# Kernel tuning notes

Hardware: AMD Instinct MI355X
Metric: run time of the kernel (lower is better)

The kernel has to match this reference:

```python
import jax, jax.numpy as jnp
import numpy as np


def setup_inputs() -> dict:
    key = jax.random.key(0)
    k1, k2, k3 = jax.random.split(key, 3)
    B, N, D = 64, 2048, 1024
    output = jax.random.normal(k1, (B, 1, D), dtype=jnp.float32)
    context = jax.random.normal(k2, (B, N, D), dtype=jnp.float32)
    # nn.Linear(2*dim, dim): weight [dim, 2*dim], bias [dim]
    W_out = jax.random.normal(k3, (D, 2 * D), dtype=jnp.float32) * (1.0 / np.sqrt(2 * D))
    b_out = jnp.zeros((D,), dtype=jnp.float32)
    return {"output": output, "context": context, "W_out": W_out, "b_out": b_out}


def reference(output, context, W_out, b_out):
    B, q, D = output.shape  # q == 1
    N = context.shape[1]
    # scores: (B, q, N) = output @ context^T
    attn = jnp.einsum('bqd,bnd->bqn', output, context)
    attn = jax.nn.softmax(attn, axis=-1)
    # mix: (B, q, D)
    mix = jnp.einsum('bqn,bnd->bqd', attn, context)
    combined = jnp.concatenate([mix, output], axis=-1)  # (B, q, 2D)
    out = jnp.tanh(jnp.einsum('bqe,de->bqd', combined, W_out) + b_out)
    return (out, attn)
```

## Files before the change

kernel.cpp:

```cpp
#include <hip/hip_runtime.h>
#include <cmath>

#define BATCH 64
#define NCTX 2048
#define DIM 1024
#define CHUNKS 16
#define ROWS_PER_CHUNK (NCTX / CHUNKS)
#define ROWS_PER_WAVE (ROWS_PER_CHUNK / 4)

__global__ __launch_bounds__(256) void attn_phase1(
    const float* __restrict__ q,
    const float* __restrict__ ctx,
    float* __restrict__ scores,
    float* __restrict__ part_m,
    float* __restrict__ part_l,
    float* __restrict__ part_o)
{
    const int blk  = blockIdx.x;
    const int b    = blk / CHUNKS;
    const int c    = blk % CHUNKS;
    const int tid  = threadIdx.x;
    const int wave = tid >> 6;
    const int lane = tid & 63;

    float4 qf[4];
    const float* qb = q + (size_t)b * DIM;
    #pragma unroll
    for (int j = 0; j < 4; ++j)
        qf[j] = *reinterpret_cast<const float4*>(qb + lane * 4 + 256 * j);

    float m = -INFINITY, l = 0.f;
    float4 o[4];
    #pragma unroll
    for (int j = 0; j < 4; ++j) o[j] = make_float4(0.f, 0.f, 0.f, 0.f);

    const int row0 = c * ROWS_PER_CHUNK + wave * ROWS_PER_WAVE;
    const float* cb = ctx + (size_t)b * NCTX * DIM;

    for (int i = 0; i < ROWS_PER_WAVE; ++i) {
        const int row = row0 + i;
        const float* cr = cb + (size_t)row * DIM + lane * 4;
        float4 cf[4];
        #pragma unroll
        for (int j = 0; j < 4; ++j)
            cf[j] = *reinterpret_cast<const float4*>(cr + 256 * j);

        float s = 0.f;
        #pragma unroll
        for (int j = 0; j < 4; ++j) {
            s += qf[j].x * cf[j].x;
            s += qf[j].y * cf[j].y;
            s += qf[j].z * cf[j].z;
            s += qf[j].w * cf[j].w;
        }
        #pragma unroll
        for (int off = 32; off >= 1; off >>= 1)
            s += __shfl_xor(s, off, 64);

        if (lane == 0) scores[(size_t)b * NCTX + row] = s;

        const float m_new = fmaxf(m, s);
        const float alpha = __expf(m - m_new);
        const float p     = __expf(s - m_new);
        l = l * alpha + p;
        #pragma unroll
        for (int j = 0; j < 4; ++j) {
            o[j].x = o[j].x * alpha + p * cf[j].x;
            o[j].y = o[j].y * alpha + p * cf[j].y;
            o[j].z = o[j].z * alpha + p * cf[j].z;
            o[j].w = o[j].w * alpha + p * cf[j].w;
        }
        m = m_new;
    }

    __shared__ float wm[4], wl[4];
    __shared__ float o_lds[4 * DIM];
    if (lane == 0) { wm[wave] = m; wl[wave] = l; }
    __syncthreads();

    const float Mb = fmaxf(fmaxf(wm[0], wm[1]), fmaxf(wm[2], wm[3]));
    float Lb = 0.f;
    #pragma unroll
    for (int w = 0; w < 4; ++w) Lb += wl[w] * __expf(wm[w] - Mb);

    const float aw = __expf(m - Mb);
    #pragma unroll
    for (int j = 0; j < 4; ++j) {
        float4 t = o[j];
        t.x *= aw; t.y *= aw; t.z *= aw; t.w *= aw;
        *reinterpret_cast<float4*>(&o_lds[wave * DIM + lane * 4 + 256 * j]) = t;
    }
    __syncthreads();

    {
        const int e = tid * 4;
        float4 s0 = *reinterpret_cast<const float4*>(&o_lds[0 * DIM + e]);
        float4 s1 = *reinterpret_cast<const float4*>(&o_lds[1 * DIM + e]);
        float4 s2 = *reinterpret_cast<const float4*>(&o_lds[2 * DIM + e]);
        float4 s3 = *reinterpret_cast<const float4*>(&o_lds[3 * DIM + e]);
        float4 r;
        r.x = s0.x + s1.x + s2.x + s3.x;
        r.y = s0.y + s1.y + s2.y + s3.y;
        r.z = s0.z + s1.z + s2.z + s3.z;
        r.w = s0.w + s1.w + s2.w + s3.w;
        *reinterpret_cast<float4*>(&part_o[((size_t)b * CHUNKS + c) * DIM + e]) = r;
    }
    if (tid == 0) {
        part_m[b * CHUNKS + c] = Mb;
        part_l[b * CHUNKS + c] = Lb;
    }
}

__global__ __launch_bounds__(256) void attn_phase2(
    const float* __restrict__ scores,
    const float* __restrict__ part_m,
    const float* __restrict__ part_l,
    const float* __restrict__ part_o,
    float* __restrict__ mix,
    float* __restrict__ attn_out)
{
    const int b = blockIdx.x;
    const int tid = threadIdx.x;

    float M = -INFINITY;
    #pragma unroll
    for (int i = 0; i < CHUNKS; ++i) M = fmaxf(M, part_m[b * CHUNKS + i]);

    float w[CHUNKS];
    float L = 0.f;
    #pragma unroll
    for (int i = 0; i < CHUNKS; ++i) {
        w[i] = __expf(part_m[b * CHUNKS + i] - M);
        L += part_l[b * CHUNKS + i] * w[i];
    }
    const float invL = 1.f / L;

    const int e = tid * 4;
    float4 acc = make_float4(0.f, 0.f, 0.f, 0.f);
    #pragma unroll
    for (int i = 0; i < CHUNKS; ++i) {
        float4 t = *reinterpret_cast<const float4*>(
            &part_o[((size_t)b * CHUNKS + i) * DIM + e]);
        acc.x += t.x * w[i];
        acc.y += t.y * w[i];
        acc.z += t.z * w[i];
        acc.w += t.w * w[i];
    }
    acc.x *= invL; acc.y *= invL; acc.z *= invL; acc.w *= invL;
    *reinterpret_cast<float4*>(&mix[(size_t)b * DIM + e]) = acc;

    for (int n = tid; n < NCTX; n += 256)
        attn_out[(size_t)b * NCTX + n] =
            __expf(scores[(size_t)b * NCTX + n] - M) * invL;
}

#define BT 8
#define DT 32
__global__ __launch_bounds__(256) void attn_phase3(
    const float* __restrict__ mix,
    const float* __restrict__ q,
    const float* __restrict__ W,
    const float* __restrict__ bias,
    float* __restrict__ out)
{
    const int d_chunk = blockIdx.x % (DIM / DT);
    const int b_chunk = blockIdx.x / (DIM / DT);
    const int d0 = d_chunk * DT;
    const int b0 = b_chunk * BT;
    const int tid  = threadIdx.x;
    const int wave = tid >> 6;
    const int lane = tid & 63;

    __shared__ float comb[BT * 2 * DIM];
    for (int i = tid; i < BT * 2 * DIM; i += 256) {
        const int bl = i >> 11;
        const int e  = i & 2047;
        comb[i] = (e < DIM) ? mix[(size_t)(b0 + bl) * DIM + e]
                            : q[(size_t)(b0 + bl) * DIM + (e - DIM)];
    }
    __syncthreads();

    const int d_base = d0 + wave * (DT / 4);
    #pragma unroll
    for (int g = 0; g < 2; ++g) {
        const int dg = d_base + g * 4;
        float acc[4][BT];
        #pragma unroll
        for (int di = 0; di < 4; ++di)
            #pragma unroll
            for (int bl = 0; bl < BT; ++bl) acc[di][bl] = 0.f;

        for (int kk = 0; kk < 2 * DIM; kk += 256) {
            float4 wv[4];
            #pragma unroll
            for (int di = 0; di < 4; ++di)
                wv[di] = *reinterpret_cast<const float4*>(
                    W + (size_t)(dg + di) * (2 * DIM) + kk + lane * 4);
            #pragma unroll
            for (int bl = 0; bl < BT; ++bl) {
                float4 cv = *reinterpret_cast<const float4*>(
                    &comb[bl * 2 * DIM + kk + lane * 4]);
                #pragma unroll
                for (int di = 0; di < 4; ++di) {
                    acc[di][bl] += wv[di].x * cv.x;
                    acc[di][bl] += wv[di].y * cv.y;
                    acc[di][bl] += wv[di].z * cv.z;
                    acc[di][bl] += wv[di].w * cv.w;
                }
            }
        }

        float myval = 0.f;
        #pragma unroll
        for (int di = 0; di < 4; ++di) {
            #pragma unroll
            for (int bl = 0; bl < BT; ++bl) {
                float v = acc[di][bl];
                #pragma unroll
                for (int off = 32; off >= 1; off >>= 1)
                    v += __shfl_xor(v, off, 64);
                if (lane == di * BT + bl) myval = v;
            }
        }
        if (lane < 32) {
            const int di = lane >> 3;
            const int bl = lane & 7;
            const int d  = dg + di;
            out[(size_t)(b0 + bl) * DIM + d] = tanhf(myval + bias[d]);
        }
    }
}

extern "C" void kernel_launch(void* const* d_in, const int* in_sizes, int n_in,
                              void* d_out, int out_size, void* d_ws, size_t ws_size,
                              hipStream_t stream) {
    const float* q    = (const float*)d_in[0];
    const float* ctx  = (const float*)d_in[1];
    const float* W    = (const float*)d_in[2];
    const float* bias = (const float*)d_in[3];

    float* out_main = (float*)d_out;
    float* attn_out = (float*)d_out + (size_t)BATCH * DIM;

    float* ws      = (float*)d_ws;
    float* scores  = ws;
    float* part_m  = scores + (size_t)BATCH * NCTX;
    float* part_l  = part_m + BATCH * CHUNKS;
    float* part_o  = part_l + BATCH * CHUNKS;
    float* mix     = part_o + (size_t)BATCH * CHUNKS * DIM;

    attn_phase1<<<BATCH * CHUNKS, 256, 0, stream>>>(q, ctx, scores,
                                                    part_m, part_l, part_o);
    attn_phase2<<<BATCH, 256, 0, stream>>>(scores, part_m, part_l, part_o,
                                           mix, attn_out);
    attn_phase3<<<(DIM / DT) * (BATCH / BT), 256, 0, stream>>>(mix, q, W, bias,
                                                               out_main);
}
```

Before: 713.7 us.

## Process two context rows per iteration, double chunks, shrink phase3 batch tile

```diff
diff --git a/kernel.cpp b/kernel.cpp
--- a/kernel.cpp
+++ b/kernel.cpp
@@ -4,7 +4,7 @@
 #define BATCH 64
 #define NCTX 2048
 #define DIM 1024
-#define CHUNKS 16
+#define CHUNKS 32
 #define ROWS_PER_CHUNK (NCTX / CHUNKS)
 #define ROWS_PER_WAVE (ROWS_PER_CHUNK / 4)
 
@@ -36,41 +36,59 @@
 
     const int row0 = c * ROWS_PER_CHUNK + wave * ROWS_PER_WAVE;
     const float* cb = ctx + (size_t)b * NCTX * DIM;
-
-    for (int i = 0; i < ROWS_PER_WAVE; ++i) {
-        const int row = row0 + i;
-        const float* cr = cb + (size_t)row * DIM + lane * 4;
-        float4 cf[4];
-        #pragma unroll
-        for (int j = 0; j < 4; ++j)
-            cf[j] = *reinterpret_cast<const float4*>(cr + 256 * j);
-
-        float s = 0.f;
+    float* sc = scores + (size_t)b * NCTX;
+
+    for (int i = 0; i < ROWS_PER_WAVE; i += 2) {
+        const int rowA = row0 + i;
+        const int rowB = rowA + 1;
+        const float* crA = cb + (size_t)rowA * DIM + lane * 4;
+        const float* crB = cb + (size_t)rowB * DIM + lane * 4;
+        float4 cfA[4], cfB[4];
         #pragma unroll
         for (int j = 0; j < 4; ++j) {
-            s += qf[j].x * cf[j].x;
-            s += qf[j].y * cf[j].y;
-            s += qf[j].z * cf[j].z;
-            s += qf[j].w * cf[j].w;
-        }
-        #pragma unroll
-        for (int off = 32; off >= 1; off >>= 1)
-            s += __shfl_xor(s, off, 64);
-
-        if (lane == 0) scores[(size_t)b * NCTX + row] = s;
-
-        const float m_new = fmaxf(m, s);
-        const float alpha = __expf(m - m_new);
-        const float p     = __expf(s - m_new);
-        l = l * alpha + p;
+            cfA[j] = *reinterpret_cast<const float4*>(crA + 256 * j);
+            cfB[j] = *reinterpret_cast<const float4*>(crB + 256 * j);
+        }
+
+        float dA[4], dB[4];
         #pragma unroll
         for (int j = 0; j < 4; ++j) {
-            o[j].x = o[j].x * alpha + p * cf[j].x;
-            o[j].y = o[j].y * alpha + p * cf[j].y;
-            o[j].z = o[j].z * alpha + p * cf[j].z;
-            o[j].w = o[j].w * alpha + p * cf[j].w;
-        }
-        m = m_new;
+            dA[j] = qf[j].x * cfA[j].x + qf[j].y * cfA[j].y
+                  + qf[j].z * cfA[j].z + qf[j].w * cfA[j].w;
+            dB[j] = qf[j].x * cfB[j].x + qf[j].y * cfB[j].y
+                  + qf[j].z * cfB[j].z + qf[j].w * cfB[j].w;
+        }
+        float s0 = (dA[0] + dA[1]) + (dA[2] + dA[3]);
+        float s1 = (dB[0] + dB[1]) + (dB[2] + dB[3]);
+
+        #pragma unroll
+        for (int off = 32; off >= 1; off >>= 1) {
+            s0 += __shfl_xor(s0, off, 64);
+            s1 += __shfl_xor(s1, off, 64);
+        }
+
+        if (lane < 2) sc[rowA + lane] = lane ? s1 : s0;
+
+        const float m_new = fmaxf(m, fmaxf(s0, s1));
+        if (m_new > m) {
+            const float a = __expf(m - m_new);
+            l *= a;
+            #pragma unroll
+            for (int j = 0; j < 4; ++j) {
+                o[j].x *= a; o[j].y *= a; o[j].z *= a; o[j].w *= a;
+            }
+            m = m_new;
+        }
+        const float p0 = __expf(s0 - m);
+        const float p1 = __expf(s1 - m);
+        l += p0 + p1;
+        #pragma unroll
+        for (int j = 0; j < 4; ++j) {
+            o[j].x += p0 * cfA[j].x + p1 * cfB[j].x;
+            o[j].y += p0 * cfA[j].y + p1 * cfB[j].y;
+            o[j].z += p0 * cfA[j].z + p1 * cfB[j].z;
+            o[j].w += p0 * cfA[j].w + p1 * cfB[j].w;
+        }
     }
 
     __shared__ float wm[4], wl[4];
@@ -154,7 +172,7 @@
             __expf(scores[(size_t)b * NCTX + n] - M) * invL;
 }
 
-#define BT 8
+#define BT 4
 #define DT 32
 __global__ __launch_bounds__(256) void attn_phase3(
     const float* __restrict__ mix,
@@ -222,9 +240,9 @@
                 if (lane == di * BT + bl) myval = v;
             }
         }
-        if (lane < 32) {
-            const int di = lane >> 3;
-            const int bl = lane & 7;
+        if (lane < 16) {
+            const int di = lane >> 2;
+            const int bl = lane & 3;
             const int d  = dg + di;
             out[(size_t)(b0 + bl) * DIM + d] = tanhf(myval + bias[d]);
         }
```

Result: no change. 711.2 us (-0.3%).
